# Performance work log

Measured on AMD Instinct MI355X. Metric: run time of the kernel, lower is better.

The kernel has to match this reference:

```python
import jax, jax.numpy as jnp
import numpy as np

NQ, NT, NC = 40000, 10000, 50000
N = NQ + NT + NC
D, H, L = 256, 8, 2
DK = D // H
DEG = 8
EPS = 1e-9


def _ln(x, g, b):
    m = x.mean(-1, keepdims=True)
    v = ((x - m) ** 2).mean(-1, keepdims=True)
    return (x - m) / jnp.sqrt(v + 1e-5) * g + b


def _attn(qh, kh, vh, src, dst, n_dst):
    # qh: [n_dst,H,DK]; kh,vh: [n_src,H,DK]; per-edge exp(clamped scaled dot) + segment sums
    s = (kh[src] * qh[dst]).sum(-1)                      # [E,H]
    s = jnp.exp(jnp.clip(s / jnp.sqrt(jnp.float32(DK)), -5.0, 5.0))
    wv = jax.ops.segment_sum(vh[src] * s[..., None], dst, num_segments=n_dst)  # [n_dst,H,DK]
    z = jax.ops.segment_sum(s, dst, num_segments=n_dst)                        # [n_dst,H]
    return wv, z


def _mk_edges(key, n_dst, n_src):
    dst = jnp.repeat(jnp.arange(n_dst, dtype=jnp.int32), DEG)
    src = jax.random.randint(key, (n_dst * DEG,), 0, n_src, dtype=jnp.int32)
    return src, dst


def setup_inputs() -> dict:
    key = jax.random.key(0)
    ks = iter(jax.random.split(key, 40))
    x = jax.random.normal(next(ks), (N, D), jnp.float32)

    def lin(fi, fo):
        return jax.random.normal(next(ks), (L, 3, fi, fo), jnp.float32) / np.sqrt(fi).astype(np.float32)

    inp = {
        'x': x,
        'Wq': lin(D, D), 'bq': jnp.zeros((L, 3, D), jnp.float32),
        'Wk': lin(D, D), 'Wv': lin(D, D),
        'Wo': lin(D, D), 'bo': jnp.zeros((L, 3, D), jnp.float32),
        'g1': jnp.ones((L, 3, D), jnp.float32), 'b1ln': jnp.zeros((L, 3, D), jnp.float32),
        'W1': lin(D, 4 * D), 'bf1': jnp.zeros((L, 3, 4 * D), jnp.float32),
        'W2': lin(4 * D, D), 'bf2': jnp.zeros((L, 3, D), jnp.float32),
        'g2': jnp.ones((L, 3, D), jnp.float32), 'b2ln': jnp.zeros((L, 3, D), jnp.float32),
    }
    sizes = (NQ, NT, NC)
    ends = (1, 2, 0)  # q<-t, t<-c, c<-q
    names = ('q', 't', 'c')
    for i, nm in enumerate(names):
        s, d = _mk_edges(next(ks), sizes[i], sizes[i])
        inp['hs_' + nm], inp['hd_' + nm] = s, d
        s, d = _mk_edges(next(ks), sizes[i], sizes[ends[i]])
        inp['ss_' + nm], inp['sd_' + nm] = s, d
        s, d = _mk_edges(next(ks), sizes[i], sizes[i])
        inp['ds_' + nm], inp['dd_' + nm] = s, d
    return inp


def reference(x, Wq, bq, Wk, Wv, Wo, bo, g1, b1ln, W1, bf1, W2, bf2, g2, b2ln,
              hs_q, hd_q, hs_t, hd_t, hs_c, hd_c,
              ss_q, sd_q, ds_q, dd_q, ss_t, sd_t, ds_t, dd_t, ss_c, sd_c, ds_c, dd_c):
    sizes = (NQ, NT, NC)
    ends = (1, 2, 0)
    homo = [(hs_q, hd_q), (hs_t, hd_t), (hs_c, hd_c)]
    het_sd = [(ss_q, sd_q), (ss_t, sd_t), (ss_c, sd_c)]
    het_dd = [(ds_q, dd_q), (ds_t, dd_t), (ds_c, dd_c)]

    for l in range(L):
        xs = [x[:NQ], x[NQ:NQ + NT], x[NQ + NT:]]
        q = [xs[i] @ Wq[l, i] + bq[l, i] for i in range(3)]
        k = [xs[i] @ Wk[l, i] for i in range(3)]
        v = [xs[i] @ Wv[l, i] for i in range(3)]
        outs = []
        for i in range(3):
            n, j = sizes[i], ends[i]
            qh = q[i].reshape(n, H, DK)
            kh = k[i].reshape(n, H, DK)
            vh = v[i].reshape(n, H, DK)
            khj = k[j].reshape(sizes[j], H, DK)
            vhj = v[j].reshape(sizes[j], H, DK)
            # homogeneous metapath graph
            wv, z = _attn(qh, kh, vh, homo[i][0], homo[i][1], n)
            o0 = wv / (z[..., None] + EPS)
            # heterogeneous metapath graph: src->dst edges use end-type k/v, dst->dst use own
            wv0, z0 = _attn(qh, khj, vhj, het_sd[i][0], het_sd[i][1], n)
            wv1, z1 = _attn(qh, kh, vh, het_dd[i][0], het_dd[i][1], n)
            o1 = (wv0 + wv1) / ((z0 + z1)[..., None] + EPS)
            acc = jnp.zeros_like(xs[i])
            for o in (o0, o1):
                h = _ln(xs[i] + o.reshape(n, D) @ Wo[l, i] + bo[l, i], g1[l, i], b1ln[l, i])
                h = _ln(h + jax.nn.relu(h @ W1[l, i] + bf1[l, i]) @ W2[l, i] + bf2[l, i], g2[l, i], b2ln[l, i])
                acc = acc + h
            outs.append(acc * 0.5)  # mean over the 2 metapaths (no_mp_attn)
        x = jnp.concatenate(outs, axis=0)
    return x
```

## Files before the change

### kernel.cpp

```cpp
#include <hip/hip_runtime.h>

#define NQn 40000
#define NTn 10000
#define NCn 50000
#define NTOT 100000
#define DIM 256
#define DEG 8

typedef __bf16 bf16x8 __attribute__((ext_vector_type(8)));
typedef float f32x4 __attribute__((ext_vector_type(4)));

#if __has_builtin(__builtin_amdgcn_exp2f)
#define EXP2F(x) __builtin_amdgcn_exp2f(x)
#else
#define EXP2F(x) exp2f(x)
#endif

static __device__ __forceinline__ float bf2f(unsigned short u) {
    union { unsigned int i; float f; } v; v.i = ((unsigned int)u) << 16; return v.f;
}
static __device__ __forceinline__ unsigned short f2bf(float f) {
    union { unsigned int i; float f; } v; v.f = f;
    unsigned int u = v.i;
    return (unsigned short)((u + 0x7fffu + ((u >> 16) & 1u)) >> 16);
}

__global__ void cvt_kernel(const float* __restrict__ in, unsigned short* __restrict__ out, int n) {
    int i = blockIdx.x * 256 + threadIdx.x;
    if (i < n) out[i] = f2bf(in[i]);
}

__global__ void transpose_cvt2(const float* __restrict__ W, unsigned short* __restrict__ WT,
                               int K, int NN, int total, int ostride, int nnoff) {
    int i = blockIdx.x * 256 + threadIdx.x;
    if (i >= total) return;
    int per = K * NN;
    int m = i / per;
    int rem = i - m * per;
    int k = rem / NN;
    int nn = rem - k * NN;
    WT[(size_t)m * ostride + (size_t)(nn + nnoff) * K + k] = f2bf(W[i]);
}

__global__ __launch_bounds__(256) void gemm_bt(
    const unsigned short* __restrict__ A,
    const unsigned short* __restrict__ BT,
    const float* __restrict__ bias,
    unsigned short* __restrict__ C,
    int M, int N, int K, int relu)
{
    __shared__ unsigned short a_lds[128 * 32];
    __shared__ unsigned short b_lds[128 * 32];
    const int tid  = threadIdx.x;
    const int w    = tid >> 6;
    const int lane = tid & 63;
    const int rb = blockIdx.x * 128;
    const int cb = blockIdx.y * 128;
    const int wrow = (w & 1) * 64;
    const int wcol = (w >> 1) * 64;
    const int q   = lane >> 4;
    const int r16 = lane & 15;

    f32x4 acc[4][4];
#pragma unroll
    for (int i = 0; i < 4; ++i)
#pragma unroll
        for (int j = 0; j < 4; ++j) acc[i][j] = f32x4{0.f, 0.f, 0.f, 0.f};

    for (int k0 = 0; k0 < K; k0 += 32) {
        __syncthreads();
#pragma unroll
        for (int it = 0; it < 2; ++it) {
            int fl  = it * 256 + tid;
            int row = fl >> 2;
            int c8  = (fl & 3) * 8;
            int arow = rb + row; if (arow > M - 1) arow = M - 1;
            const unsigned short* ga = A  + (size_t)arow * K + k0 + c8;
            const unsigned short* gb = BT + (size_t)(cb + row) * K + k0 + c8;
            unsigned short* la = &a_lds[(size_t)(it * 256 + (tid & ~63)) * 8];
            unsigned short* lb = &b_lds[(size_t)(it * 256 + (tid & ~63)) * 8];
            __builtin_amdgcn_global_load_lds((const __attribute__((address_space(1))) void*)ga,
                                             (__attribute__((address_space(3))) void*)la, 16, 0, 0);
            __builtin_amdgcn_global_load_lds((const __attribute__((address_space(1))) void*)gb,
                                             (__attribute__((address_space(3))) void*)lb, 16, 0, 0);
        }
        __syncthreads();
        bf16x8 af[4], bfr[4];
#pragma unroll
        for (int mi = 0; mi < 4; ++mi)
            af[mi] = *(const bf16x8*)&a_lds[(wrow + mi * 16 + r16) * 32 + q * 8];
#pragma unroll
        for (int ni = 0; ni < 4; ++ni)
            bfr[ni] = *(const bf16x8*)&b_lds[(wcol + ni * 16 + r16) * 32 + q * 8];
#pragma unroll
        for (int mi = 0; mi < 4; ++mi)
#pragma unroll
            for (int ni = 0; ni < 4; ++ni)
                acc[mi][ni] = __builtin_amdgcn_mfma_f32_16x16x32_bf16(af[mi], bfr[ni], acc[mi][ni], 0, 0, 0);
    }

#pragma unroll
    for (int mi = 0; mi < 4; ++mi) {
#pragma unroll
        for (int ni = 0; ni < 4; ++ni) {
            int col = cb + wcol + ni * 16 + r16;
            float bv = bias ? bias[col] : 0.f;
#pragma unroll
            for (int rr = 0; rr < 4; ++rr) {
                int row = rb + wrow + mi * 16 + q * 4 + rr;
                if (row < M) {
                    float v = acc[mi][ni][rr] + bv;
                    if (relu && v < 0.f) v = 0.f;
                    C[(size_t)row * N + col] = f2bf(v);
                }
            }
        }
    }
}

__global__ __launch_bounds__(256, 2) void ffn_fused(
    const unsigned short* __restrict__ hbp,
    const unsigned short* __restrict__ w1p,
    const float* __restrict__ b1p,
    const unsigned short* __restrict__ w2p,
    const float* __restrict__ b2p,
    unsigned short* __restrict__ fout,
    int M)
{
    __shared__ __align__(16) unsigned short w1_lds[2][32 * 256];
    __shared__ __align__(16) unsigned short w2_lds[2][256 * 32];
    __shared__ __align__(16) unsigned short u_lds[4][32 * 32];

    const int tid  = threadIdx.x;
    const int w    = tid >> 6;
    const int lane = tid & 63;
    const int q    = lane >> 4;
    const int r16  = lane & 15;
    const int row0 = blockIdx.x * 128 + w * 32;

    bf16x8 hf[2][8];
#pragma unroll
    for (int nj = 0; nj < 2; ++nj) {
        int rrow = row0 + nj * 16 + r16;
        if (rrow > M - 1) rrow = M - 1;
        const unsigned short* hr = hbp + (size_t)rrow * DIM;
#pragma unroll
        for (int kk = 0; kk < 8; ++kk)
            hf[nj][kk] = *(const bf16x8*)&hr[kk * 32 + q * 8];
    }

    f32x4 acc[2][16];
#pragma unroll
    for (int mj = 0; mj < 2; ++mj)
#pragma unroll
        for (int nf = 0; nf < 16; ++nf) acc[mj][nf] = f32x4{0.f, 0.f, 0.f, 0.f};

    auto stage = [&](int c, int buf) {
#pragma unroll
        for (int it = 0; it < 4; ++it) {
            int fl = it * 256 + tid;
            int n = fl >> 5, c16 = fl & 31;
            int sc = (c16 & 24) | ((c16 ^ n) & 7);
            const unsigned short* g = w1p + (size_t)(c * 32 + n) * 256 + sc * 8;
            unsigned short* l = &w1_lds[buf][(size_t)(it * 256 + (tid & ~63)) * 8];
            __builtin_amdgcn_global_load_lds((const __attribute__((address_space(1))) void*)g,
                                             (__attribute__((address_space(3))) void*)l, 16, 0, 0);
        }
#pragma unroll
        for (int it = 0; it < 4; ++it) {
            int fl = it * 256 + tid;
            int n = fl >> 2, c4 = fl & 3;
            int sc = c4 ^ ((n >> 1) & 3);
            const unsigned short* g = w2p + (size_t)n * 1024 + c * 32 + sc * 8;
            unsigned short* l = &w2_lds[buf][(size_t)(it * 256 + (tid & ~63)) * 8];
            __builtin_amdgcn_global_load_lds((const __attribute__((address_space(1))) void*)g,
                                             (__attribute__((address_space(3))) void*)l, 16, 0, 0);
        }
    };

    stage(0, 0);
    __syncthreads();

    unsigned short* ub = u_lds[w];

    for (int c = 0; c < 32; ++c) {
        int buf = c & 1;
        if (c + 1 < 32) stage(c + 1, buf ^ 1);

        const unsigned short* w1b = w1_lds[buf];
        f32x4 au[2][2];
#pragma unroll
        for (int mi = 0; mi < 2; ++mi)
#pragma unroll
            for (int nj = 0; nj < 2; ++nj) au[mi][nj] = f32x4{0.f, 0.f, 0.f, 0.f};
#pragma unroll
        for (int kk = 0; kk < 8; ++kk) {
#pragma unroll
            for (int mi = 0; mi < 2; ++mi) {
                int nrow = mi * 16 + r16;
                int ck = kk * 4 + q;
                int cks = (ck & 24) | ((ck ^ nrow) & 7);
                bf16x8 a = *(const bf16x8*)&w1b[nrow * 256 + cks * 8];
#pragma unroll
                for (int nj = 0; nj < 2; ++nj)
                    au[mi][nj] = __builtin_amdgcn_mfma_f32_16x16x32_bf16(a, hf[nj][kk], au[mi][nj], 0, 0, 0);
            }
        }

#pragma unroll
        for (int mi = 0; mi < 2; ++mi) {
            float bv[4];
#pragma unroll
            for (int rr = 0; rr < 4; ++rr)
                bv[rr] = b1p[c * 32 + mi * 16 + q * 4 + rr];
#pragma unroll
            for (int nj = 0; nj < 2; ++nj) {
                int row = nj * 16 + r16;
                int sw = (row >> 1) & 3;
                int chunk = (mi * 2 + (q >> 1)) ^ sw;
                int byteoff = row * 64 + chunk * 16 + (q & 1) * 8;
                ushort4 pk;
                pk.x = f2bf(fmaxf(au[mi][nj][0] + bv[0], 0.f));
                pk.y = f2bf(fmaxf(au[mi][nj][1] + bv[1], 0.f));
                pk.z = f2bf(fmaxf(au[mi][nj][2] + bv[2], 0.f));
                pk.w = f2bf(fmaxf(au[mi][nj][3] + bv[3], 0.f));
                *(ushort4*)((char*)ub + byteoff) = pk;
            }
        }

        const unsigned short* w2b = w2_lds[buf];
        bf16x8 aU[2];
#pragma unroll
        for (int mj = 0; mj < 2; ++mj) {
            int row = mj * 16 + r16;
            int qs = q ^ ((row >> 1) & 3);
            aU[mj] = *(const bf16x8*)((const char*)ub + row * 64 + qs * 16);
        }
#pragma unroll
        for (int nf = 0; nf < 16; ++nf) {
            int n = nf * 16 + r16;
            int qs = q ^ ((n >> 1) & 3);
            bf16x8 b = *(const bf16x8*)&w2b[n * 32 + qs * 8];
#pragma unroll
            for (int mj = 0; mj < 2; ++mj)
                acc[mj][nf] = __builtin_amdgcn_mfma_f32_16x16x32_bf16(aU[mj], b, acc[mj][nf], 0, 0, 0);
        }
        __syncthreads();
    }

#pragma unroll
    for (int nf = 0; nf < 16; ++nf) {
        int col = nf * 16 + r16;
        float bv = b2p[col];
#pragma unroll
        for (int mj = 0; mj < 2; ++mj) {
#pragma unroll
            for (int rr = 0; rr < 4; ++rr) {
                int row = row0 + mj * 16 + q * 4 + rr;
                if (row < M) fout[(size_t)row * DIM + col] = f2bf(acc[mj][nf][rr] + bv);
            }
        }
    }
}

__device__ __forceinline__ void attn_accum(
    const unsigned short* __restrict__ kvb,
    const int4 s0, const int4 s1, int off_s, int hc,
    const float qv[4], float wv[4], float& z)
{
    const int sidx[8] = {s0.x, s0.y, s0.z, s0.w, s1.x, s1.y, s1.z, s1.w};
    const float CLAMP = 7.2134752f;
#pragma unroll
    for (int e = 0; e < DEG; ++e) {
        size_t basep = ((size_t)(off_s + sidx[e]) * 512) + hc;
        ushort4 k4 = *(const ushort4*)&kvb[basep];
        float dot = qv[0] * bf2f(k4.x) + qv[1] * bf2f(k4.y) + qv[2] * bf2f(k4.z) + qv[3] * bf2f(k4.w);
        dot += __shfl_xor(dot, 1);
        dot += __shfl_xor(dot, 2);
        dot += __shfl_xor(dot, 4);
        dot = fminf(fmaxf(dot, -CLAMP), CLAMP);
        float wgt = EXP2F(dot);
        ushort4 v4 = *(const ushort4*)&kvb[basep + 256];
        wv[0] += wgt * bf2f(v4.x);
        wv[1] += wgt * bf2f(v4.y);
        wv[2] += wgt * bf2f(v4.z);
        wv[3] += wgt * bf2f(v4.w);
        z += wgt;
    }
}

__global__ __launch_bounds__(256) void attn_kernel(
    const unsigned short* __restrict__ qc,
    const unsigned short* __restrict__ kvb,
    const int* __restrict__ src_h,
    const int* __restrict__ src_s,
    const int* __restrict__ src_d,
    unsigned short* __restrict__ o01,
    int rc, int off_d, int off_j)
{
    int widx = (int)((blockIdx.x * 256 + threadIdx.x) >> 6);
    if (widx >= rc) return;
    int lane = threadIdx.x & 63;
    int hc = (lane >> 3) * 32 + (lane & 7) * 4;
    const float PRESCALE = 0.17677669529663687f * 1.4426950408889634f;
    float qv[4];
    {
        ushort4 t4 = *(const ushort4*)&qc[(size_t)widx * DIM + hc];
        qv[0] = bf2f(t4.x) * PRESCALE; qv[1] = bf2f(t4.y) * PRESCALE;
        qv[2] = bf2f(t4.z) * PRESCALE; qv[3] = bf2f(t4.w) * PRESCALE;
    }
    int4 h0 = *(const int4*)&src_h[widx * DEG];
    int4 h1 = *(const int4*)&src_h[widx * DEG + 4];
    int4 ss0 = *(const int4*)&src_s[widx * DEG];
    int4 ss1 = *(const int4*)&src_s[widx * DEG + 4];
    int4 d0 = *(const int4*)&src_d[widx * DEG];
    int4 d1 = *(const int4*)&src_d[widx * DEG + 4];

    size_t ob = (size_t)widx * DIM + hc;

    float wv[4] = {0.f, 0.f, 0.f, 0.f}; float z = 0.f;
    attn_accum(kvb, h0, h1, off_d, hc, qv, wv, z);
    float inv = 1.f / (z + 1e-9f);
    o01[ob + 0] = f2bf(wv[0] * inv); o01[ob + 1] = f2bf(wv[1] * inv);
    o01[ob + 2] = f2bf(wv[2] * inv); o01[ob + 3] = f2bf(wv[3] * inv);

    wv[0] = wv[1] = wv[2] = wv[3] = 0.f; z = 0.f;
    attn_accum(kvb, ss0, ss1, off_j, hc, qv, wv, z);
    attn_accum(kvb, d0, d1, off_d, hc, qv, wv, z);
    inv = 1.f / (z + 1e-9f);
    size_t ob1 = ob + (size_t)rc * DIM;
    o01[ob1 + 0] = f2bf(wv[0] * inv); o01[ob1 + 1] = f2bf(wv[1] * inv);
    o01[ob1 + 2] = f2bf(wv[2] * inv); o01[ob1 + 3] = f2bf(wv[3] * inv);
}

__global__ __launch_bounds__(256) void ln1_kernel(
    const float* __restrict__ xres_f, const unsigned short* __restrict__ xres_b,
    const unsigned short* __restrict__ t,
    const float* __restrict__ g, const float* __restrict__ b,
    unsigned short* __restrict__ hb,
    int rc, int goff)
{
    int row = (int)((blockIdx.x * 256 + threadIdx.x) >> 6);
    int n2 = 2 * rc;
    if (row >= n2) return;
    int lane = threadIdx.x & 63;
    int dstrow = row < rc ? row : row - rc;
    size_t gbase = (size_t)(goff + dstrow) * DIM + lane * 4;
    size_t lbase = (size_t)row * DIM + lane * 4;
    float pre[4];
#pragma unroll
    for (int j = 0; j < 4; ++j) {
        float xr = xres_f ? xres_f[gbase + j] : bf2f(xres_b[gbase + j]);
        pre[j] = xr + bf2f(t[lbase + j]);
    }
    float s = 0.f, sq = 0.f;
#pragma unroll
    for (int j = 0; j < 4; ++j) { s += pre[j]; sq += pre[j] * pre[j]; }
#pragma unroll
    for (int m = 1; m < 64; m <<= 1) { s += __shfl_xor(s, m); sq += __shfl_xor(sq, m); }
    float mean = s * (1.f / 256.f);
    float var = sq * (1.f / 256.f) - mean * mean;
    float rstd = rsqrtf(var + 1e-5f);
#pragma unroll
    for (int j = 0; j < 4; ++j) {
        int col = lane * 4 + j;
        float hv = (pre[j] - mean) * rstd * g[col] + b[col];
        hb[lbase + j] = f2bf(hv);
    }
}

__global__ __launch_bounds__(256) void ln2_final(
    const unsigned short* __restrict__ hb, const unsigned short* __restrict__ f,
    const float* __restrict__ g, const float* __restrict__ b,
    unsigned short* __restrict__ xb_out,
    float* __restrict__ fout,
    int rc, int goff)
{
    int row = (int)((blockIdx.x * 256 + threadIdx.x) >> 6);
    if (row >= rc) return;
    int lane = threadIdx.x & 63;
    size_t lb0 = (size_t)row * DIM + lane * 4;
    size_t lb1 = (size_t)(rc + row) * DIM + lane * 4;
    size_t gbase = (size_t)(goff + row) * DIM + lane * 4;
    float p0[4], p1[4];
#pragma unroll
    for (int j = 0; j < 4; ++j) {
        p0[j] = bf2f(hb[lb0 + j]) + bf2f(f[lb0 + j]);
        p1[j] = bf2f(hb[lb1 + j]) + bf2f(f[lb1 + j]);
    }
    float s0 = 0.f, q0 = 0.f, s1 = 0.f, q1 = 0.f;
#pragma unroll
    for (int j = 0; j < 4; ++j) {
        s0 += p0[j]; q0 += p0[j] * p0[j];
        s1 += p1[j]; q1 += p1[j] * p1[j];
    }
#pragma unroll
    for (int m = 1; m < 64; m <<= 1) {
        s0 += __shfl_xor(s0, m); q0 += __shfl_xor(q0, m);
        s1 += __shfl_xor(s1, m); q1 += __shfl_xor(q1, m);
    }
    float m0 = s0 * (1.f / 256.f), m1 = s1 * (1.f / 256.f);
    float r0 = rsqrtf(q0 * (1.f / 256.f) - m0 * m0 + 1e-5f);
    float r1 = rsqrtf(q1 * (1.f / 256.f) - m1 * m1 + 1e-5f);
#pragma unroll
    for (int j = 0; j < 4; ++j) {
        int col = lane * 4 + j;
        float ga = g[col], ba = b[col];
        float h20 = (p0[j] - m0) * r0 * ga + ba;
        float h21 = (p1[j] - m1) * r1 * ga + ba;
        float val = (h20 + h21) * 0.5f;
        if (xb_out) xb_out[gbase + j] = f2bf(val);
        if (fout)   fout[gbase + j] = val;
    }
}

extern "C" void kernel_launch(void* const* d_in, const int* in_sizes, int n_in,
                              void* d_out, int out_size, void* d_ws, size_t ws_size,
                              hipStream_t stream) {
    const float* x0  = (const float*)d_in[0];
    const float* Wq  = (const float*)d_in[1];
    const float* bq  = (const float*)d_in[2];
    const float* Wk  = (const float*)d_in[3];
    const float* Wv  = (const float*)d_in[4];
    const float* Wo  = (const float*)d_in[5];
    const float* bo  = (const float*)d_in[6];
    const float* g1  = (const float*)d_in[7];
    const float* b1  = (const float*)d_in[8];
    const float* W1  = (const float*)d_in[9];
    const float* bf1 = (const float*)d_in[10];
    const float* W2  = (const float*)d_in[11];
    const float* bf2 = (const float*)d_in[12];
    const float* g2  = (const float*)d_in[13];
    const float* b2  = (const float*)d_in[14];
    const int* hs[3]  = {(const int*)d_in[15], (const int*)d_in[21], (const int*)d_in[27]};
    const int* ssx[3] = {(const int*)d_in[17], (const int*)d_in[23], (const int*)d_in[29]};
    const int* dsx[3] = {(const int*)d_in[19], (const int*)d_in[25], (const int*)d_in[31]};
    float* out = (float*)d_out;

    char* base = (char*)d_ws;
    size_t off = 0;
    auto carve = [&](size_t bytes) -> void* {
        void* r = base + off;
        off += (bytes + 255) & ~(size_t)255;
        return r;
    };
    unsigned short* WqT  = (unsigned short*)carve((size_t)6 * 65536 * 2);
    unsigned short* WkvT = (unsigned short*)carve((size_t)6 * 131072 * 2);
    unsigned short* WoT  = (unsigned short*)carve((size_t)6 * 65536 * 2);
    unsigned short* W1T  = (unsigned short*)carve((size_t)6 * 262144 * 2);
    unsigned short* W2T  = (unsigned short*)carve((size_t)6 * 262144 * 2);
    unsigned short* xb   = (unsigned short*)carve((size_t)NTOT * DIM * 2);
    unsigned short* kvb  = (unsigned short*)carve((size_t)NTOT * 512 * 2);

    size_t avail = (ws_size > off + 8192) ? (ws_size - off - 8192) : 0;
    long rmax = (long)(avail / 3072);
    int R = (int)(rmax & ~63L);
    if (R < 1024)  R = 1024;
    if (R > 50048) R = 50048;

    unsigned short* o01  = (unsigned short*)carve((size_t)2 * R * DIM * 2);
    unsigned short* tfb  = (unsigned short*)carve((size_t)2 * R * DIM * 2);
    unsigned short* hbb  = (unsigned short*)carve((size_t)2 * R * DIM * 2);
    unsigned short* qc   = tfb;

    {
        int tot = 6 * 65536;
        dim3 g((tot + 255) / 256);
        transpose_cvt2<<<g, 256, 0, stream>>>(Wq, WqT, 256, 256, tot, 65536, 0);
        transpose_cvt2<<<g, 256, 0, stream>>>(Wk, WkvT, 256, 256, tot, 131072, 0);
        transpose_cvt2<<<g, 256, 0, stream>>>(Wv, WkvT, 256, 256, tot, 131072, 256);
        transpose_cvt2<<<g, 256, 0, stream>>>(Wo, WoT, 256, 256, tot, 65536, 0);
        int tot2 = 6 * 262144;
        dim3 g2d((tot2 + 255) / 256);
        transpose_cvt2<<<g2d, 256, 0, stream>>>(W1, W1T, 256, 1024, tot2, 262144, 0);
        transpose_cvt2<<<g2d, 256, 0, stream>>>(W2, W2T, 1024, 256, tot2, 262144, 0);
        int totx = NTOT * DIM;
        cvt_kernel<<<dim3((totx + 255) / 256), 256, 0, stream>>>(x0, xb, totx);
    }

    const int offs[3] = {0, NQn, NQn + NTn};
    const int ns[3]   = {NQn, NTn, NCn};
    const int ends[3] = {1, 2, 0};

    auto gemm = [&](const unsigned short* A, const unsigned short* BT, const float* bias,
                    unsigned short* C, int M, int N, int K, int relu) {
        dim3 g((M + 127) / 128, N / 128);
        gemm_bt<<<g, 256, 0, stream>>>(A, BT, bias, C, M, N, K, relu);
    };

    for (int l = 0; l < 2; ++l) {
        for (int i = 0; i < 3; ++i) {
            int m = l * 3 + i;
            gemm(xb + (size_t)offs[i] * DIM, WkvT + (size_t)m * 131072, nullptr,
                 kvb + (size_t)offs[i] * 512, ns[i], 512, 256, 0);
        }
        for (int i = 0; i < 3; ++i) {
            int m = l * 3 + i;
            for (int r0 = 0; r0 < ns[i]; r0 += R) {
                int rc = ns[i] - r0 < R ? ns[i] - r0 : R;
                int goff = offs[i] + r0;
                gemm(xb + (size_t)goff * DIM, WqT + (size_t)m * 65536, bq + (size_t)m * 256,
                     qc, rc, 256, 256, 0);
                attn_kernel<<<dim3((rc + 3) / 4), 256, 0, stream>>>(
                    qc, kvb,
                    hs[i] + (size_t)r0 * DEG, ssx[i] + (size_t)r0 * DEG, dsx[i] + (size_t)r0 * DEG,
                    o01, rc, offs[i], offs[ends[i]]);
                gemm(o01, WoT + (size_t)m * 65536, bo + (size_t)m * 256, tfb, 2 * rc, 256, 256, 0);
                ln1_kernel<<<dim3((2 * rc + 3) / 4), 256, 0, stream>>>(
                    l == 0 ? x0 : nullptr, l == 0 ? nullptr : xb, tfb,
                    g1 + (size_t)m * 256, b1 + (size_t)m * 256, hbb, rc, goff);
                ffn_fused<<<dim3((2 * rc + 127) / 128), 256, 0, stream>>>(
                    hbb, W1T + (size_t)m * 262144, bf1 + (size_t)m * 1024,
                    W2T + (size_t)m * 262144, bf2 + (size_t)m * 256, tfb, 2 * rc);
                ln2_final<<<dim3((rc + 3) / 4), 256, 0, stream>>>(
                    hbb, tfb, g2 + (size_t)m * 256, b2 + (size_t)m * 256,
                    l == 0 ? xb : nullptr, l == 1 ? out : nullptr,
                    rc, goff);
            }
        }
    }
}
```

Before: 2.877 ms.

## Pre-pack FFN weights into MFMA fragment order and load directly from global

W1 and W2 are repacked once into a layout where each lane's bf16x8 MFMA operand is contiguous, and the fused FFN kernel reads these fragments straight from global memory or cache. This removes the LDS double-buffer staging, the swizzle index math and the per-chunk __syncthreads. In exchange, every wave issues its own global loads for the shared weights with no LDS reuse across the block's four waves, which depends on L1/L2 hit rates and may expose load latency to the MFMAs. LDS use drops sharply, which could allow higher occupancy.

```diff
diff --git a/kernel.cpp b/kernel.cpp
--- a/kernel.cpp
+++ b/kernel.cpp
@@ -40,6 +40,33 @@
     int k = rem / NN;
     int nn = rem - k * NN;
     WT[(size_t)m * ostride + (size_t)(nn + nnoff) * K + k] = f2bf(W[i]);
+}
+
+__global__ void pack_w1(const float* __restrict__ W, unsigned short* __restrict__ P, int total) {
+    int i = blockIdx.x * 256 + threadIdx.x;
+    if (i >= total) return;
+    int j  = i & 7;
+    int l  = (i >> 3) & 63;
+    int mi = (i >> 9) & 1;
+    int kk = (i >> 10) & 7;
+    int c  = (i >> 13) & 31;
+    int m  = i >> 18;
+    int ucol = c * 32 + mi * 16 + (l & 15);
+    int k    = kk * 32 + (l >> 4) * 8 + j;
+    P[i] = f2bf(W[((size_t)m * 256 + k) * 1024 + ucol]);
+}
+
+__global__ void pack_w2(const float* __restrict__ W, unsigned short* __restrict__ P, int total) {
+    int i = blockIdx.x * 256 + threadIdx.x;
+    if (i >= total) return;
+    int j  = i & 7;
+    int l  = (i >> 3) & 63;
+    int nf = (i >> 9) & 15;
+    int c  = (i >> 13) & 31;
+    int m  = i >> 18;
+    int ocol = nf * 16 + (l & 15);
+    int u    = c * 32 + (l >> 4) * 8 + j;
+    P[i] = f2bf(W[((size_t)m * 1024 + u) * 256 + ocol]);
 }
 
 __global__ __launch_bounds__(256) void gemm_bt(
@@ -120,15 +147,13 @@
 
 __global__ __launch_bounds__(256, 2) void ffn_fused(
     const unsigned short* __restrict__ hbp,
-    const unsigned short* __restrict__ w1p,
+    const unsigned short* __restrict__ w1f,
     const float* __restrict__ b1p,
-    const unsigned short* __restrict__ w2p,
+    const unsigned short* __restrict__ w2f,
     const float* __restrict__ b2p,
     unsigned short* __restrict__ fout,
     int M)
 {
-    __shared__ __align__(16) unsigned short w1_lds[2][32 * 256];
-    __shared__ __align__(16) unsigned short w2_lds[2][256 * 32];
     __shared__ __align__(16) unsigned short u_lds[4][32 * 32];
 
     const int tid  = threadIdx.x;
@@ -155,39 +180,11 @@
 #pragma unroll
         for (int nf = 0; nf < 16; ++nf) acc[mj][nf] = f32x4{0.f, 0.f, 0.f, 0.f};
 
-    auto stage = [&](int c, int buf) {
-#pragma unroll
-        for (int it = 0; it < 4; ++it) {
-            int fl = it * 256 + tid;
-            int n = fl >> 5, c16 = fl & 31;
-            int sc = (c16 & 24) | ((c16 ^ n) & 7);
-            const unsigned short* g = w1p + (size_t)(c * 32 + n) * 256 + sc * 8;
-            unsigned short* l = &w1_lds[buf][(size_t)(it * 256 + (tid & ~63)) * 8];
-            __builtin_amdgcn_global_load_lds((const __attribute__((address_space(1))) void*)g,
-                                             (__attribute__((address_space(3))) void*)l, 16, 0, 0);
-        }
-#pragma unroll
-        for (int it = 0; it < 4; ++it) {
-            int fl = it * 256 + tid;
-            int n = fl >> 2, c4 = fl & 3;
-            int sc = c4 ^ ((n >> 1) & 3);
-            const unsigned short* g = w2p + (size_t)n * 1024 + c * 32 + sc * 8;
-            unsigned short* l = &w2_lds[buf][(size_t)(it * 256 + (tid & ~63)) * 8];
-            __builtin_amdgcn_global_load_lds((const __attribute__((address_space(1))) void*)g,
-                                             (__attribute__((address_space(3))) void*)l, 16, 0, 0);
-        }
-    };
-
-    stage(0, 0);
-    __syncthreads();
-
+    const bf16x8* w1v = (const bf16x8*)w1f + lane;
+    const bf16x8* w2v = (const bf16x8*)w2f + lane;
     unsigned short* ub = u_lds[w];
 
     for (int c = 0; c < 32; ++c) {
-        int buf = c & 1;
-        if (c + 1 < 32) stage(c + 1, buf ^ 1);
-
-        const unsigned short* w1b = w1_lds[buf];
         f32x4 au[2][2];
 #pragma unroll
         for (int mi = 0; mi < 2; ++mi)
@@ -197,10 +194,7 @@
         for (int kk = 0; kk < 8; ++kk) {
 #pragma unroll
             for (int mi = 0; mi < 2; ++mi) {
-                int nrow = mi * 16 + r16;
-                int ck = kk * 4 + q;
-                int cks = (ck & 24) | ((ck ^ nrow) & 7);
-                bf16x8 a = *(const bf16x8*)&w1b[nrow * 256 + cks * 8];
+                bf16x8 a = w1v[(size_t)((c * 8 + kk) * 2 + mi) * 64];
 #pragma unroll
                 for (int nj = 0; nj < 2; ++nj)
                     au[mi][nj] = __builtin_amdgcn_mfma_f32_16x16x32_bf16(a, hf[nj][kk], au[mi][nj], 0, 0, 0);
@@ -228,7 +222,6 @@
             }
         }
 
-        const unsigned short* w2b = w2_lds[buf];
         bf16x8 aU[2];
 #pragma unroll
         for (int mj = 0; mj < 2; ++mj) {
@@ -238,14 +231,11 @@
         }
 #pragma unroll
         for (int nf = 0; nf < 16; ++nf) {
-            int n = nf * 16 + r16;
-            int qs = q ^ ((n >> 1) & 3);
-            bf16x8 b = *(const bf16x8*)&w2b[n * 32 + qs * 8];
+            bf16x8 b = w2v[(size_t)(c * 16 + nf) * 64];
 #pragma unroll
             for (int mj = 0; mj < 2; ++mj)
                 acc[mj][nf] = __builtin_amdgcn_mfma_f32_16x16x32_bf16(aU[mj], b, acc[mj][nf], 0, 0, 0);
         }
-        __syncthreads();
     }
 
 #pragma unroll
@@ -447,8 +437,8 @@
     unsigned short* WqT  = (unsigned short*)carve((size_t)6 * 65536 * 2);
     unsigned short* WkvT = (unsigned short*)carve((size_t)6 * 131072 * 2);
     unsigned short* WoT  = (unsigned short*)carve((size_t)6 * 65536 * 2);
-    unsigned short* W1T  = (unsigned short*)carve((size_t)6 * 262144 * 2);
-    unsigned short* W2T  = (unsigned short*)carve((size_t)6 * 262144 * 2);
+    unsigned short* W1F  = (unsigned short*)carve((size_t)6 * 262144 * 2);
+    unsigned short* W2F  = (unsigned short*)carve((size_t)6 * 262144 * 2);
     unsigned short* xb   = (unsigned short*)carve((size_t)NTOT * DIM * 2);
     unsigned short* kvb  = (unsigned short*)carve((size_t)NTOT * 512 * 2);
 
@@ -472,8 +462,8 @@
         transpose_cvt2<<<g, 256, 0, stream>>>(Wo, WoT, 256, 256, tot, 65536, 0);
         int tot2 = 6 * 262144;
         dim3 g2d((tot2 + 255) / 256);
-        transpose_cvt2<<<g2d, 256, 0, stream>>>(W1, W1T, 256, 1024, tot2, 262144, 0);
-        transpose_cvt2<<<g2d, 256, 0, stream>>>(W2, W2T, 1024, 256, tot2, 262144, 0);
+        pack_w1<<<g2d, 256, 0, stream>>>(W1, W1F, tot2);
+        pack_w2<<<g2d, 256, 0, stream>>>(W2, W2F, tot2);
         int totx = NTOT * DIM;
         cvt_kernel<<<dim3((totx + 255) / 256), 256, 0, stream>>>(x0, xb, totx);
     }
@@ -510,8 +500,8 @@
                     l == 0 ? x0 : nullptr, l == 0 ? nullptr : xb, tfb,
                     g1 + (size_t)m * 256, b1 + (size_t)m * 256, hbb, rc, goff);
                 ffn_fused<<<dim3((2 * rc + 127) / 128), 256, 0, stream>>>(
-                    hbb, W1T + (size_t)m * 262144, bf1 + (size_t)m * 1024,
-                    W2T + (size_t)m * 262144, bf2 + (size_t)m * 256, tfb, 2 * rc);
+                    hbb, W1F + (size_t)m * 262144, bf1 + (size_t)m * 1024,
+                    W2F + (size_t)m * 262144, bf2 + (size_t)m * 256, tfb, 2 * rc);
                 ln2_final<<<dim3((rc + 3) / 4), 256, 0, stream>>>(
                     hbb, tfb, g2 + (size_t)m * 256, b2 + (size_t)m * 256,
                     l == 0 ? xb : nullptr, l == 1 ? out : nullptr,
```

After: 3.852 ms. 1.34x slower.
